# Kernel optimization log

Hardware: AMD Instinct MI355X
Metric: run time of the kernel (lower is better)

## Reference

```python
import jax, jax.numpy as jnp
import numpy as np

# 4-bit symmetric narrow-range weight quant (Brevitas Int-WeightPerTensorFloat style)
# and 4-bit unsigned activation quant after ReLU (QuantReLU style), with
# straight-through rounding so the same code is valid for the bwd reference.

W_QMAX = 7.0    # 2**(4-1)-1, narrow range symmetric int4: [-7, 7]
A_QMAX = 15.0   # unsigned 4-bit: [0, 15]
EPS = 1e-8


def _round_ste(x):
    return x + jax.lax.stop_gradient(jnp.round(x) - x)


def quant_weight(W):
    # per-tensor scale from max abs value
    scale = jnp.max(jnp.abs(W)) / W_QMAX + EPS
    q = jnp.clip(_round_ste(W / scale), -W_QMAX, W_QMAX)
    return q * scale


def quant_relu(x, scale):
    # ReLU fused with unsigned 4-bit quant/dequant, per-tensor learned scale
    q = jnp.clip(_round_ste(jax.nn.relu(x) / scale), 0.0, A_QMAX)
    return q * scale


def setup_inputs() -> dict:
    key = jax.random.key(0)
    k = jax.random.split(key, 4)
    B = 65536
    x = jax.random.normal(k[0], (B, 28, 28), dtype=jnp.float32)
    W1 = jax.random.normal(k[1], (512, 784), dtype=jnp.float32) * 0.05
    W2 = jax.random.normal(k[2], (512, 512), dtype=jnp.float32) * 0.05
    W3 = jax.random.normal(k[3], (10, 512), dtype=jnp.float32) * 0.05
    s1 = jnp.float32(1.0)  # QuantReLU activation scales (learned params)
    s2 = jnp.float32(1.0)
    return {"x": x, "W1": W1, "W2": W2, "W3": W3, "s1": s1, "s2": s2}


def reference(x, W1, W2, W3, s1, s2):
    h = x.reshape(x.shape[0], -1)                       # flatten [B, 784]
    h = h @ quant_weight(W1).T                          # QuantLinear 784->512
    h = quant_relu(h, s1)                               # QuantReLU
    h = h @ quant_weight(W2).T                          # QuantLinear 512->512
    h = quant_relu(h, s2)                               # QuantReLU
    logits = h @ quant_weight(W3).T                     # QuantLinear 512->10
    return logits
```

## Files before the change

### kernel.cpp

```cpp
#include <hip/hip_runtime.h>
#include <hip/hip_fp16.h>

typedef _Float16 f16;
typedef _Float16 f16x4 __attribute__((ext_vector_type(4)));
typedef _Float16 f16x8 __attribute__((ext_vector_type(8)));
typedef float f32x4 __attribute__((ext_vector_type(4)));
typedef int i32x4 __attribute__((ext_vector_type(4)));

#define MFMA16(a, b, c) __builtin_amdgcn_mfma_f32_16x16x32_f16((a), (b), (c), 0, 0, 0)
#define MFMAI8(a, b, c) __builtin_amdgcn_mfma_i32_16x16x64_i8((a), (b), (c), 0, 0, 0)

#define FLAG_CAP (1024 * 1024)
#define FLAG_TOL 1e-3f

__device__ __forceinline__ void gld16(const void* g, void* l) {
    __builtin_amdgcn_global_load_lds(
        (const __attribute__((address_space(1))) unsigned int*)g,
        (__attribute__((address_space(3))) unsigned int*)l,
        16, 0, 0);
}


__global__ void k_zero(float* p, int* cnt) {
    if (threadIdx.x < 3) p[threadIdx.x] = 0.f;
    if (threadIdx.x == 3) { cnt[0] = 0; cnt[1] = 0; }
}

__global__ void k_absmax(const float* __restrict__ w, int n, float* __restrict__ out) {
    float m = 0.f;
    int stride = gridDim.x * blockDim.x;
    for (int i = blockIdx.x * blockDim.x + threadIdx.x; i < n; i += stride)
        m = fmaxf(m, fabsf(w[i]));
    #pragma unroll
    for (int o = 32; o > 0; o >>= 1) m = fmaxf(m, __shfl_down(m, o));
    __shared__ float sm[4];
    int lane = threadIdx.x & 63, wv = threadIdx.x >> 6;
    if (lane == 0) sm[wv] = m;
    __syncthreads();
    if (threadIdx.x == 0) {
        float mm = fmaxf(fmaxf(sm[0], sm[1]), fmaxf(sm[2], sm[3]));
        atomicMax((unsigned int*)out, __float_as_uint(mm));
    }
}

__global__ void k_quantw1(const float* __restrict__ w, const float* __restrict__ wmax,
                          f16* __restrict__ q1, float* __restrict__ wdq,
                          f16* __restrict__ q1h) {
    int i = blockIdx.x * blockDim.x + threadIdx.x;
    if (i >= 512 * 832) return;
    int n = i / 832, k = i - n * 832;
    float v = 0.f;
    if (k < 784) {
        float s = wmax[0] / 7.0f + 1e-8f;
        v = rintf(w[n * 784 + k] / s);
        v = fminf(fmaxf(v, -7.f), 7.f);
        q1[n * 784 + k] = (f16)v;
        wdq[n * 784 + k] = v * s;
    }
    q1h[(size_t)n * 832 + k] = (f16)v;
}

__global__ void k_quantw2(const float* __restrict__ w, const float* __restrict__ wmax,
                          signed char* __restrict__ q, float* __restrict__ wdq, int n) {
    float s = wmax[0] / 7.0f + 1e-8f;
    int i = blockIdx.x * blockDim.x + threadIdx.x;
    if (i < n) {
        float v = rintf(w[i] / s);
        v = fminf(fmaxf(v, -7.f), 7.f);
        q[i] = (signed char)v;
        if (wdq) wdq[i] = v * s;
    }
}

__global__ void k_quantw3(const float* __restrict__ w, const float* __restrict__ wmax,
                          signed char* __restrict__ q) {
    float s = wmax[0] / 7.0f + 1e-8f;
    int i = blockIdx.x * blockDim.x + threadIdx.x;
    if (i < 16 * 512) {
        float v = 0.f;
        if (i < 10 * 512) {
            v = rintf(w[i] / s);
            v = fminf(fmaxf(v, -7.f), 7.f);
        }
        q[i] = (signed char)v;
    }
}


__global__ void k_prep(const float* __restrict__ X, f16* __restrict__ Xs) {
    int row = blockIdx.x;
    int p = threadIdx.x;
    if (p >= 208) return;
    f16x4 h0 = (f16x4){0, 0, 0, 0}, h1 = (f16x4){0, 0, 0, 0};
    if (p < 196) {
        float4 v = *reinterpret_cast<const float4*>(X + (size_t)row * 784 + p * 4);
        float vv[4] = {v.x, v.y, v.z, v.w};
        #pragma unroll
        for (int j = 0; j < 4; ++j) {
            f16 c0 = (f16)vv[j];
            h0[j] = c0;
            h1[j] = (f16)(vv[j] - (float)c0);
        }
    }
    *reinterpret_cast<f16x4*>(Xs + (size_t)row * 1664 + p * 4) = h0;
    *reinterpret_cast<f16x4*>(Xs + (size_t)row * 1664 + 832 + p * 4) = h1;
}


__global__ __launch_bounds__(256, 3) void k_gemm1h(
    const f16* __restrict__ A, const f16* __restrict__ B,
    const float* __restrict__ wmax, const float* __restrict__ s1p,
    signed char* __restrict__ A1, int* __restrict__ flagCnt, unsigned* __restrict__ flagList)
{
    constexpr int KA = 1664;
    constexpr int KB = 832;
    constexpr int NT = 13;
    __shared__ __align__(16) f16 Ah[128 * 64];
    __shared__ __align__(16) f16 Al[128 * 64];
    __shared__ __align__(16) f16 Bt[128 * 64];

    const int t = threadIdx.x;
    const int lane = t & 63, w = t >> 6;
    const int wr = w >> 1, wc = w & 1;

    const int bid = blockIdx.x;
    const int lg = (bid & 7) * 256 + (bid >> 3);
    const int n0 = (lg & 3) * 128;
    const int row0 = (lg >> 2) * 128;

    f32x4 acc[4][4];
    #pragma unroll
    for (int m = 0; m < 4; ++m)
        #pragma unroll
        for (int n = 0; n < 4; ++n) acc[m][n] = (f32x4){0.f, 0.f, 0.f, 0.f};

    const int lr = lane >> 3;
    const int lc = (((lane & 7) ^ (lane >> 3)) * 8);
    const f16* Ahb = A + (size_t)(row0 + lr) * KA + lc;
    const f16* Alb = A + (size_t)(row0 + lr) * KA + 832 + lc;
    const f16* Bb  = B + (size_t)(n0 + lr) * KB + lc;

    for (int tt = 0; tt < NT; ++tt) {
        const int k0 = tt * 64;
        #pragma unroll
        for (int i = 0; i < 4; ++i) {
            int ch = w * 4 + i;
            gld16(Ahb + (size_t)ch * 8 * KA + k0, &Ah[ch * 512]);
            gld16(Alb + (size_t)ch * 8 * KA + k0, &Al[ch * 512]);
            gld16(Bb  + (size_t)ch * 8 * KB + k0, &Bt[ch * 512]);
        }
        __syncthreads();

        #pragma unroll
        for (int kk = 0; kk < 2; ++kk) {
            int kb = kk * 32 + (lane >> 4) * 8;
            int ksw = kb ^ ((lane & 7) << 3);
            f16x8 bf[4], fh[4], fl[4];
            #pragma unroll
            for (int n = 0; n < 4; ++n)
                bf[n] = *reinterpret_cast<const f16x8*>(&Bt[(wc * 64 + n * 16 + (lane & 15)) * 64 + ksw]);
            #pragma unroll
            for (int m = 0; m < 4; ++m) {
                fh[m] = *reinterpret_cast<const f16x8*>(&Ah[(wr * 64 + m * 16 + (lane & 15)) * 64 + ksw]);
                fl[m] = *reinterpret_cast<const f16x8*>(&Al[(wr * 64 + m * 16 + (lane & 15)) * 64 + ksw]);
            }
            #pragma unroll
            for (int m = 0; m < 4; ++m)
                #pragma unroll
                for (int n = 0; n < 4; ++n) {
                    acc[m][n] = MFMA16(fh[m], bf[n], acc[m][n]);
                    acc[m][n] = MFMA16(fl[m], bf[n], acc[m][n]);
                }
        }
        __syncthreads();
    }

    float sw = wmax[0] / 7.0f + 1e-8f;
    float s1v = s1p[0];
    #pragma unroll
    for (int m = 0; m < 4; ++m)
        #pragma unroll
        for (int n = 0; n < 4; ++n)
            #pragma unroll
            for (int j = 0; j < 4; ++j) {
                int row = row0 + wr * 64 + m * 16 + (lane >> 4) * 4 + j;
                int col = n0 + wc * 64 + n * 16 + (lane & 15);
                float h = sw * acc[m][n][j];
                float r = fmaxf(h, 0.f) / s1v;
                float qv = fminf(rintf(r), 15.f);
                A1[(size_t)row * 512 + col] = (signed char)qv;
                float fr = r - floorf(r);
                if (fabsf(fr - 0.5f) < FLAG_TOL) {
                    int p = atomicAdd(flagCnt, 1);
                    if (p < FLAG_CAP) flagList[p] = (unsigned)(row * 512 + col);
                }
            }
}


__global__ __launch_bounds__(256, 4) void k_gemm2i(
    const signed char* __restrict__ A, const signed char* __restrict__ B,
    const float* __restrict__ wmax, const float* __restrict__ s1p, const float* __restrict__ s2p,
    signed char* __restrict__ A2, int* __restrict__ flagCnt, unsigned* __restrict__ flagList)
{
    constexpr int KP = 512;
    constexpr int NT = 4;
    __shared__ __align__(16) signed char As[128 * 128];
    __shared__ __align__(16) signed char Bs[128 * 128];

    const int t = threadIdx.x;
    const int lane = t & 63, w = t >> 6;
    const int wr = w >> 1, wc = w & 1;

    const int bid = blockIdx.x;
    const int lg = (bid & 7) * 256 + (bid >> 3);
    const int n0 = (lg & 3) * 128;
    const int row0 = (lg >> 2) * 128;

    i32x4 acc[4][4];
    #pragma unroll
    for (int m = 0; m < 4; ++m)
        #pragma unroll
        for (int n = 0; n < 4; ++n) acc[m][n] = (i32x4){0, 0, 0, 0};

    const int lr = lane >> 3;
    const int lcb = (((lane & 7) ^ (lane >> 3)) * 16);
    const signed char* Ab = A + (size_t)(row0 + lr) * KP + lcb;
    const signed char* Bb = B + (size_t)(n0 + lr) * KP + lcb;

    for (int tt = 0; tt < NT; ++tt) {
        const int k0 = tt * 128;
        #pragma unroll
        for (int i = 0; i < 4; ++i) {
            int ch = w * 4 + i;
            gld16(Ab + (size_t)ch * 8 * KP + k0, &As[ch * 1024]);
            gld16(Bb + (size_t)ch * 8 * KP + k0, &Bs[ch * 1024]);
        }
        __syncthreads();

        #pragma unroll
        for (int kk = 0; kk < 2; ++kk) {
            int sl = kk * 4 + (lane >> 4);
            int slw = (sl ^ (lane & 7)) * 16;
            i32x4 bf[4], af[4];
            #pragma unroll
            for (int n = 0; n < 4; ++n)
                bf[n] = *reinterpret_cast<const i32x4*>(&Bs[(wc * 64 + n * 16 + (lane & 15)) * 128 + slw]);
            #pragma unroll
            for (int m = 0; m < 4; ++m)
                af[m] = *reinterpret_cast<const i32x4*>(&As[(wr * 64 + m * 16 + (lane & 15)) * 128 + slw]);
            #pragma unroll
            for (int m = 0; m < 4; ++m)
                #pragma unroll
                for (int n = 0; n < 4; ++n)
                    acc[m][n] = MFMAI8(af[m], bf[n], acc[m][n]);
        }
        __syncthreads();
    }

    double cs = (double)s1p[0] * (double)(wmax[0] / 7.0f + 1e-8f);
    double s2v = (double)s2p[0];
    #pragma unroll
    for (int m = 0; m < 4; ++m)
        #pragma unroll
        for (int n = 0; n < 4; ++n)
            #pragma unroll
            for (int j = 0; j < 4; ++j) {
                int row = row0 + wr * 64 + m * 16 + (lane >> 4) * 4 + j;
                int col = n0 + wc * 64 + n * 16 + (lane & 15);
                double r = fmax((double)acc[m][n][j] * cs, 0.0) / s2v;
                double qv = fmin(rint(r), 15.0);
                A2[(size_t)row * 512 + col] = (signed char)qv;
                double fr = r - floor(r);
                if (fabs(fr - 0.5) < (double)FLAG_TOL && r < 16.0) {
                    int p = atomicAdd(flagCnt, 1);
                    if (p < FLAG_CAP) flagList[p] = (unsigned)(row * 512 + col);
                }
            }
}


__global__ __launch_bounds__(256) void k_gemm1s(
    const float* __restrict__ X, const f16* __restrict__ Q1,
    const float* __restrict__ wmax, const float* __restrict__ s1p,
    signed char* __restrict__ A1, int* __restrict__ flagCnt, unsigned* __restrict__ flagList)
{
    __shared__ __align__(16) f16 As0[128][72];
    __shared__ __align__(16) f16 As1[128][72];
    __shared__ __align__(16) f16 Bs[128][72];

    const int t = threadIdx.x;
    const int row0 = blockIdx.y * 128;
    const int n0 = blockIdx.x * 128;
    const int lane = t & 63, wv = t >> 6;
    const int wr = wv >> 1, wc = wv & 1;

    f32x4 acc[4][4];
    #pragma unroll
    for (int m = 0; m < 4; ++m)
        #pragma unroll
        for (int n = 0; n < 4; ++n) acc[m][n] = (f32x4){0.f, 0.f, 0.f, 0.f};

    for (int k0 = 0; k0 < 784; k0 += 64) {
        #pragma unroll
        for (int i = 0; i < 8; ++i) {
            int f = t + 256 * i;
            int r = f >> 4, c = f & 15;
            int gk = k0 + c * 4;
            float4 v = make_float4(0.f, 0.f, 0.f, 0.f);
            if (gk < 784)
                v = *reinterpret_cast<const float4*>(X + (size_t)(row0 + r) * 784 + gk);
            float vv[4] = {v.x, v.y, v.z, v.w};
            f16x4 h0, h1;
            #pragma unroll
            for (int j = 0; j < 4; ++j) {
                f16 c0 = (f16)vv[j];
                h0[j] = c0;
                h1[j] = (f16)(vv[j] - (float)c0);
            }
            *reinterpret_cast<f16x4*>(&As0[r][c * 4]) = h0;
            *reinterpret_cast<f16x4*>(&As1[r][c * 4]) = h1;
        }
        #pragma unroll
        for (int i = 0; i < 4; ++i) {
            int f = t + 256 * i;
            int r = f >> 3, c = f & 7;
            int gk = k0 + c * 8;
            uint4 u = make_uint4(0u, 0u, 0u, 0u);
            if (gk < 784)
                u = *reinterpret_cast<const uint4*>(Q1 + (size_t)(n0 + r) * 784 + gk);
            *reinterpret_cast<uint4*>(&Bs[r][c * 8]) = u;
        }
        __syncthreads();

        #pragma unroll
        for (int kk = 0; kk < 2; ++kk) {
            int kb = kk * 32 + (lane >> 4) * 8;
            f16x8 bf[4], a0[4], a1f[4];
            #pragma unroll
            for (int n = 0; n < 4; ++n)
                bf[n] = *reinterpret_cast<const f16x8*>(&Bs[wc * 64 + n * 16 + (lane & 15)][kb]);
            #pragma unroll
            for (int m = 0; m < 4; ++m) {
                a0[m]  = *reinterpret_cast<const f16x8*>(&As0[wr * 64 + m * 16 + (lane & 15)][kb]);
                a1f[m] = *reinterpret_cast<const f16x8*>(&As1[wr * 64 + m * 16 + (lane & 15)][kb]);
            }
            #pragma unroll
            for (int m = 0; m < 4; ++m)
                #pragma unroll
                for (int n = 0; n < 4; ++n) {
                    acc[m][n] = MFMA16(a0[m],  bf[n], acc[m][n]);
                    acc[m][n] = MFMA16(a1f[m], bf[n], acc[m][n]);
                }
        }
        __syncthreads();
    }

    float sw = wmax[0] / 7.0f + 1e-8f;
    float s1v = s1p[0];
    #pragma unroll
    for (int m = 0; m < 4; ++m)
        #pragma unroll
        for (int n = 0; n < 4; ++n)
            #pragma unroll
            for (int j = 0; j < 4; ++j) {
                int row = row0 + wr * 64 + m * 16 + (lane >> 4) * 4 + j;
                int col = n0 + wc * 64 + n * 16 + (lane & 15);
                float h = sw * acc[m][n][j];
                float r = fmaxf(h, 0.f) / s1v;
                float qv = fminf(rintf(r), 15.f);
                A1[(size_t)row * 512 + col] = (signed char)qv;
                float fr = r - floorf(r);
                if (fabsf(fr - 0.5f) < FLAG_TOL) {
                    int p = atomicAdd(flagCnt, 1);
                    if (p < FLAG_CAP) flagList[p] = (unsigned)(row * 512 + col);
                }
            }
}


__global__ void k_fixup1(const float* __restrict__ X, const float* __restrict__ W1dq,
                         const float* __restrict__ s1p,
                         const int* __restrict__ flagCnt, const unsigned* __restrict__ flagList,
                         signed char* __restrict__ A1)
{
    int tid = blockIdx.x * blockDim.x + threadIdx.x;
    int nthr = gridDim.x * blockDim.x;
    int n = flagCnt[0];
    if (n > FLAG_CAP) n = FLAG_CAP;
    float s1 = s1p[0];
    for (int i = tid; i < n; i += nthr) {
        unsigned idx = flagList[i];
        int row = (int)(idx >> 9), col = (int)(idx & 511);
        const float* xr = X + (size_t)row * 784;
        const float* wr = W1dq + (size_t)col * 784;
        float acc = 0.f;
        for (int k = 0; k < 784; ++k)
            acc = fmaf(xr[k], wr[k], acc);
        float tq = fmaxf(acc, 0.f) / s1;
        float code = fminf(rintf(tq), 15.f);
        A1[(size_t)row * 512 + col] = (signed char)code;
    }
}

__global__ void k_fixup2(const signed char* __restrict__ A1, const float* __restrict__ W2dq,
                         const float* __restrict__ s1p, const float* __restrict__ s2p,
                         const int* __restrict__ flagCnt, const unsigned* __restrict__ flagList,
                         signed char* __restrict__ A2)
{
    int tid = blockIdx.x * blockDim.x + threadIdx.x;
    int nthr = gridDim.x * blockDim.x;
    int n = flagCnt[0];
    if (n > FLAG_CAP) n = FLAG_CAP;
    float s1 = s1p[0], s2 = s2p[0];
    for (int i = tid; i < n; i += nthr) {
        unsigned idx = flagList[i];
        int row = (int)(idx >> 9), col = (int)(idx & 511);
        const signed char* ar = A1 + (size_t)row * 512;
        const float* wr = W2dq + (size_t)col * 512;
        float acc = 0.f;
        for (int k = 0; k < 512; ++k) {
            float adq = (float)ar[k] * s1;
            acc = fmaf(adq, wr[k], acc);
        }
        float tq = fmaxf(acc, 0.f) / s2;
        float code = fminf(rintf(tq), 15.f);
        A2[(size_t)row * 512 + col] = (signed char)code;
    }
}


__global__ __launch_bounds__(256) void k_gemm3i(
    const signed char* __restrict__ A2, const signed char* __restrict__ Q3,
    const float* __restrict__ wmax, const float* __restrict__ s2p,
    float* __restrict__ Out)
{
    __shared__ __align__(16) signed char As[256][80];
    __shared__ __align__(16) signed char Bs[16][80];

    const int t = threadIdx.x;
    const int row0 = blockIdx.x * 256;
    const int lane = t & 63, wv = t >> 6;

    i32x4 acc[4];
    #pragma unroll
    for (int m = 0; m < 4; ++m) acc[m] = (i32x4){0, 0, 0, 0};

    for (int k0 = 0; k0 < 512; k0 += 64) {
        #pragma unroll
        for (int i = 0; i < 4; ++i) {
            int f = t + 256 * i;
            int r = f >> 2, c = f & 3;
            *reinterpret_cast<uint4*>(&As[r][c * 16]) =
                *reinterpret_cast<const uint4*>(A2 + (size_t)(row0 + r) * 512 + k0 + c * 16);
        }
        if (t < 64) {
            int r = t >> 2, c = t & 3;
            *reinterpret_cast<uint4*>(&Bs[r][c * 16]) =
                *reinterpret_cast<const uint4*>(Q3 + (size_t)r * 512 + k0 + c * 16);
        }
        __syncthreads();

        i32x4 bf = *reinterpret_cast<const i32x4*>(&Bs[lane & 15][(lane >> 4) * 16]);
        #pragma unroll
        for (int m = 0; m < 4; ++m) {
            i32x4 af = *reinterpret_cast<const i32x4*>(&As[wv * 64 + m * 16 + (lane & 15)][(lane >> 4) * 16]);
            acc[m] = MFMAI8(af, bf, acc[m]);
        }
        __syncthreads();
    }

    double cs = (double)s2p[0] * (double)(wmax[0] / 7.0f + 1e-8f);
    #pragma unroll
    for (int m = 0; m < 4; ++m)
        #pragma unroll
        for (int j = 0; j < 4; ++j) {
            int row = row0 + wv * 64 + m * 16 + (lane >> 4) * 4 + j;
            int col = lane & 15;
            if (col < 10)
                Out[(size_t)row * 10 + col] = (float)((double)acc[m][j] * cs);
        }
}


extern "C" void kernel_launch(void* const* d_in, const int* in_sizes, int n_in,
                              void* d_out, int out_size, void* d_ws, size_t ws_size,
                              hipStream_t stream)
{
    (void)in_sizes; (void)n_in; (void)out_size;

    const float* X  = (const float*)d_in[0];
    const float* W1 = (const float*)d_in[1];
    const float* W2 = (const float*)d_in[2];
    const float* W3 = (const float*)d_in[3];
    const float* s1 = (const float*)d_in[4];
    const float* s2 = (const float*)d_in[5];
    float* Out = (float*)d_out;

    char* ws = (char*)d_ws;
    float* maxes        = (float*)ws;
    int*   cnts         = (int*)(ws + 16);
    f16*   q1           = (f16*)(ws + 4096);
    signed char* q2i    = (signed char*)(ws + (size_t)(1u << 20));
    signed char* q3i    = (signed char*)(ws + (size_t)(1u << 20) + 300000);
    f16*   q1h          = (f16*)(ws + (size_t)(2u << 20));
    float* w1dq         = (float*)(ws + (size_t)(4u << 20));
    float* w2dq         = (float*)(ws + (size_t)(6u << 20));
    signed char* a1     = (signed char*)(ws + (size_t)(8u << 20));
    signed char* a2     = (signed char*)(ws + (size_t)(40u << 20));
    unsigned* fl1       = (unsigned*)(ws + (size_t)(72u << 20));
    unsigned* fl2       = (unsigned*)(ws + (size_t)(76u << 20));
    f16*   Xs           = (f16*)(ws + (size_t)(80u << 20));

    const bool big = ws_size >= ((size_t)300 << 20);

    k_zero<<<1, 64, 0, stream>>>(maxes, cnts);
    k_absmax<<<256, 256, 0, stream>>>(W1, 512 * 784, maxes + 0);
    k_absmax<<<256, 256, 0, stream>>>(W2, 512 * 512, maxes + 1);
    k_absmax<<<8, 256, 0, stream>>>(W3, 10 * 512, maxes + 2);
    k_quantw1<<<(512 * 832 + 255) / 256, 256, 0, stream>>>(W1, maxes + 0, q1, w1dq, q1h);
    k_quantw2<<<(512 * 512 + 255) / 256, 256, 0, stream>>>(W2, maxes + 1, q2i, w2dq, 512 * 512);
    k_quantw3<<<(16 * 512 + 255) / 256, 256, 0, stream>>>(W3, maxes + 2, q3i);

    if (big) {
        k_prep<<<65536, 256, 0, stream>>>(X, Xs);
        k_gemm1h<<<2048, 256, 0, stream>>>(Xs, q1h, maxes + 0, s1, a1, cnts + 0, fl1);
    } else {
        k_gemm1s<<<dim3(4, 512), 256, 0, stream>>>(X, q1, maxes + 0, s1, a1, cnts + 0, fl1);
    }
    k_fixup1<<<512, 256, 0, stream>>>(X, w1dq, s1, cnts + 0, fl1, a1);
    k_gemm2i<<<2048, 256, 0, stream>>>(a1, q2i, maxes + 1, s1, s2, a2, cnts + 1, fl2);
    k_fixup2<<<512, 256, 0, stream>>>(a1, w2dq, s1, s2, cnts + 1, fl2, a2);
    k_gemm3i<<<256, 256, 0, stream>>>(a2, q3i, maxes + 2, s2, Out);
}
```

Baseline: 669.5 us.

## Fuse fp16 split of X into GEMM1 and widen both GEMMs to full-N tiles

Removes the separate prep kernel that wrote a split hi/lo fp16 copy of X to global memory. GEMM1 now loads fp32 X directly, converts it to hi/lo fp16 in registers and writes it into double-buffered, swizzled LDS, prefetching the next K tile while the MFMAs run. Both GEMM1 and the int8 GEMM2 now use 512-thread blocks that compute a 128x512 output tile, so each A tile is loaded once instead of four times, and A is double-buffered with explicit waitcnt and barrier control. The costs are a large LDS footprint that limits occupancy, more accumulator registers per thread, and dropping the small-workspace fallback path.

Result: faster. 624.4 us (-6.7%).

```diff
diff --git a/kernel.cpp b/kernel.cpp
--- a/kernel.cpp
+++ b/kernel.cpp
@@ -12,6 +12,9 @@
 
 #define FLAG_CAP (1024 * 1024)
 #define FLAG_TOL 1e-3f
+
+#define SBAR()   __builtin_amdgcn_s_barrier()
+#define SCHEDB() __builtin_amdgcn_sched_barrier(0)
 
 __device__ __forceinline__ void gld16(const void* g, void* l) {
     __builtin_amdgcn_global_load_lds(
@@ -44,8 +47,7 @@
 }
 
 __global__ void k_quantw1(const float* __restrict__ w, const float* __restrict__ wmax,
-                          f16* __restrict__ q1, float* __restrict__ wdq,
-                          f16* __restrict__ q1h) {
+                          float* __restrict__ wdq, f16* __restrict__ q1h) {
     int i = blockIdx.x * blockDim.x + threadIdx.x;
     if (i >= 512 * 832) return;
     int n = i / 832, k = i - n * 832;
@@ -54,7 +56,6 @@
         float s = wmax[0] / 7.0f + 1e-8f;
         v = rintf(w[n * 784 + k] / s);
         v = fminf(fmaxf(v, -7.f), 7.f);
-        q1[n * 784 + k] = (f16)v;
         wdq[n * 784 + k] = v * s;
     }
     q1h[(size_t)n * 832 + k] = (f16)v;
@@ -87,92 +88,108 @@
 }
 
 
-__global__ void k_prep(const float* __restrict__ X, f16* __restrict__ Xs) {
-    int row = blockIdx.x;
-    int p = threadIdx.x;
-    if (p >= 208) return;
-    f16x4 h0 = (f16x4){0, 0, 0, 0}, h1 = (f16x4){0, 0, 0, 0};
-    if (p < 196) {
-        float4 v = *reinterpret_cast<const float4*>(X + (size_t)row * 784 + p * 4);
-        float vv[4] = {v.x, v.y, v.z, v.w};
-        #pragma unroll
-        for (int j = 0; j < 4; ++j) {
-            f16 c0 = (f16)vv[j];
-            h0[j] = c0;
-            h1[j] = (f16)(vv[j] - (float)c0);
-        }
-    }
-    *reinterpret_cast<f16x4*>(Xs + (size_t)row * 1664 + p * 4) = h0;
-    *reinterpret_cast<f16x4*>(Xs + (size_t)row * 1664 + 832 + p * 4) = h1;
-}
-
-
-__global__ __launch_bounds__(256, 3) void k_gemm1h(
-    const f16* __restrict__ A, const f16* __restrict__ B,
+__global__ __launch_bounds__(512, 2) void k_gemm1F(
+    const float* __restrict__ X, const f16* __restrict__ B,
     const float* __restrict__ wmax, const float* __restrict__ s1p,
     signed char* __restrict__ A1, int* __restrict__ flagCnt, unsigned* __restrict__ flagList)
 {
-    constexpr int KA = 1664;
-    constexpr int KB = 832;
     constexpr int NT = 13;
-    __shared__ __align__(16) f16 Ah[128 * 64];
-    __shared__ __align__(16) f16 Al[128 * 64];
-    __shared__ __align__(16) f16 Bt[128 * 64];
+    __shared__ __align__(16) f16 Ah[2][128 * 64];
+    __shared__ __align__(16) f16 Al[2][128 * 64];
+    __shared__ __align__(16) f16 Bt[512 * 64];
 
     const int t = threadIdx.x;
     const int lane = t & 63, w = t >> 6;
-    const int wr = w >> 1, wc = w & 1;
-
-    const int bid = blockIdx.x;
-    const int lg = (bid & 7) * 256 + (bid >> 3);
-    const int n0 = (lg & 3) * 128;
-    const int row0 = (lg >> 2) * 128;
-
-    f32x4 acc[4][4];
+    const int wr = w >> 2, wc = w & 3;
+    const int l15 = lane & 15, l4 = lane >> 4;
+    const int row0 = blockIdx.x * 128;
+
+    f32x4 acc[4][8];
     #pragma unroll
     for (int m = 0; m < 4; ++m)
         #pragma unroll
-        for (int n = 0; n < 4; ++n) acc[m][n] = (f32x4){0.f, 0.f, 0.f, 0.f};
+        for (int n = 0; n < 8; ++n) acc[m][n] = (f32x4){0.f, 0.f, 0.f, 0.f};
 
     const int lr = lane >> 3;
-    const int lc = (((lane & 7) ^ (lane >> 3)) * 8);
-    const f16* Ahb = A + (size_t)(row0 + lr) * KA + lc;
-    const f16* Alb = A + (size_t)(row0 + lr) * KA + 832 + lc;
-    const f16* Bb  = B + (size_t)(n0 + lr) * KB + lc;
-
+    const int lc = ((lane & 7) ^ lr) * 8;
+    const f16* Bb = B + (size_t)lr * 832 + lc;
+
+    float4 av[4];
+    auto LOADA = [&](int tn) {
+        #pragma unroll
+        for (int i = 0; i < 4; ++i) {
+            int f = t + 512 * i;
+            int r = f >> 4, s = f & 15;
+            int gk = tn * 64 + s * 4;
+            av[i] = make_float4(0.f, 0.f, 0.f, 0.f);
+            if (gk < 784)
+                av[i] = *reinterpret_cast<const float4*>(X + (size_t)(row0 + r) * 784 + gk);
+        }
+    };
+    auto WRITEA = [&](int buf) {
+        #pragma unroll
+        for (int i = 0; i < 4; ++i) {
+            int f = t + 512 * i;
+            int r = f >> 4, s = f & 15;
+            float vv[4] = {av[i].x, av[i].y, av[i].z, av[i].w};
+            f16x4 h0, h1;
+            #pragma unroll
+            for (int j = 0; j < 4; ++j) {
+                f16 c0 = (f16)vv[j];
+                h0[j] = c0;
+                h1[j] = (f16)(vv[j] - (float)c0);
+            }
+            int ad = r * 64 + ((s * 4) ^ ((r & 7) << 3));
+            *reinterpret_cast<f16x4*>(&Ah[buf][ad]) = h0;
+            *reinterpret_cast<f16x4*>(&Al[buf][ad]) = h1;
+        }
+    };
+
+    LOADA(0);
+    asm volatile("s_waitcnt vmcnt(0)" ::: "memory");
+    WRITEA(0);
+
+    int cur = 0;
     for (int tt = 0; tt < NT; ++tt) {
-        const int k0 = tt * 64;
-        #pragma unroll
-        for (int i = 0; i < 4; ++i) {
-            int ch = w * 4 + i;
-            gld16(Ahb + (size_t)ch * 8 * KA + k0, &Ah[ch * 512]);
-            gld16(Alb + (size_t)ch * 8 * KA + k0, &Al[ch * 512]);
-            gld16(Bb  + (size_t)ch * 8 * KB + k0, &Bt[ch * 512]);
-        }
-        __syncthreads();
+        #pragma unroll
+        for (int i = 0; i < 8; ++i) {
+            int ch = w * 8 + i;
+            gld16(Bb + (size_t)ch * 8 * 832 + tt * 64, &Bt[ch * 512]);
+        }
+        SCHEDB();
+        int tn = (tt + 1 < NT) ? tt + 1 : tt;
+        LOADA(tn);
+        SCHEDB();
+        asm volatile("s_waitcnt vmcnt(4)" ::: "memory");
+        asm volatile("s_waitcnt lgkmcnt(0)" ::: "memory");
+        SBAR();
 
         #pragma unroll
         for (int kk = 0; kk < 2; ++kk) {
-            int kb = kk * 32 + (lane >> 4) * 8;
+            int kb = kk * 32 + l4 * 8;
             int ksw = kb ^ ((lane & 7) << 3);
-            f16x8 bf[4], fh[4], fl[4];
-            #pragma unroll
-            for (int n = 0; n < 4; ++n)
-                bf[n] = *reinterpret_cast<const f16x8*>(&Bt[(wc * 64 + n * 16 + (lane & 15)) * 64 + ksw]);
+            f16x8 fh[4], fl_[4], bf[8];
             #pragma unroll
             for (int m = 0; m < 4; ++m) {
-                fh[m] = *reinterpret_cast<const f16x8*>(&Ah[(wr * 64 + m * 16 + (lane & 15)) * 64 + ksw]);
-                fl[m] = *reinterpret_cast<const f16x8*>(&Al[(wr * 64 + m * 16 + (lane & 15)) * 64 + ksw]);
+                fh[m]  = *reinterpret_cast<const f16x8*>(&Ah[cur][(wr * 64 + m * 16 + l15) * 64 + ksw]);
+                fl_[m] = *reinterpret_cast<const f16x8*>(&Al[cur][(wr * 64 + m * 16 + l15) * 64 + ksw]);
             }
+            #pragma unroll
+            for (int n = 0; n < 8; ++n)
+                bf[n] = *reinterpret_cast<const f16x8*>(&Bt[(wc * 128 + n * 16 + l15) * 64 + ksw]);
             #pragma unroll
             for (int m = 0; m < 4; ++m)
                 #pragma unroll
-                for (int n = 0; n < 4; ++n) {
-                    acc[m][n] = MFMA16(fh[m], bf[n], acc[m][n]);
-                    acc[m][n] = MFMA16(fl[m], bf[n], acc[m][n]);
+                for (int n = 0; n < 8; ++n) {
+                    acc[m][n] = MFMA16(fh[m],  bf[n], acc[m][n]);
+                    acc[m][n] = MFMA16(fl_[m], bf[n], acc[m][n]);
                 }
         }
-        __syncthreads();
+
+        asm volatile("s_waitcnt vmcnt(0)" ::: "memory");
+        WRITEA(cur ^ 1);
+        SBAR();
+        cur ^= 1;
     }
 
     float sw = wmax[0] / 7.0f + 1e-8f;
@@ -180,11 +197,11 @@
     #pragma unroll
     for (int m = 0; m < 4; ++m)
         #pragma unroll
-        for (int n = 0; n < 4; ++n)
+        for (int n = 0; n < 8; ++n)
             #pragma unroll
             for (int j = 0; j < 4; ++j) {
-                int row = row0 + wr * 64 + m * 16 + (lane >> 4) * 4 + j;
-                int col = n0 + wc * 64 + n * 16 + (lane & 15);
+                int row = row0 + wr * 64 + m * 16 + l4 * 4 + j;
+                int col = wc * 128 + n * 16 + l15;
                 float h = sw * acc[m][n][j];
                 float r = fmaxf(h, 0.f) / s1v;
                 float qv = fminf(rintf(r), 15.f);
@@ -198,64 +215,76 @@
 }
 
 
-__global__ __launch_bounds__(256, 4) void k_gemm2i(
+__global__ __launch_bounds__(512, 2) void k_gemm2F(
     const signed char* __restrict__ A, const signed char* __restrict__ B,
     const float* __restrict__ wmax, const float* __restrict__ s1p, const float* __restrict__ s2p,
     signed char* __restrict__ A2, int* __restrict__ flagCnt, unsigned* __restrict__ flagList)
 {
-    constexpr int KP = 512;
     constexpr int NT = 4;
-    __shared__ __align__(16) signed char As[128 * 128];
-    __shared__ __align__(16) signed char Bs[128 * 128];
+    __shared__ __align__(16) signed char As[2][128 * 128];
+    __shared__ __align__(16) signed char Bs[512 * 128];
 
     const int t = threadIdx.x;
     const int lane = t & 63, w = t >> 6;
-    const int wr = w >> 1, wc = w & 1;
-
-    const int bid = blockIdx.x;
-    const int lg = (bid & 7) * 256 + (bid >> 3);
-    const int n0 = (lg & 3) * 128;
-    const int row0 = (lg >> 2) * 128;
-
-    i32x4 acc[4][4];
+    const int wr = w >> 2, wc = w & 3;
+    const int l15 = lane & 15, l4 = lane >> 4;
+    const int row0 = blockIdx.x * 128;
+
+    i32x4 acc[4][8];
     #pragma unroll
     for (int m = 0; m < 4; ++m)
         #pragma unroll
-        for (int n = 0; n < 4; ++n) acc[m][n] = (i32x4){0, 0, 0, 0};
+        for (int n = 0; n < 8; ++n) acc[m][n] = (i32x4){0, 0, 0, 0};
 
     const int lr = lane >> 3;
-    const int lcb = (((lane & 7) ^ (lane >> 3)) * 16);
-    const signed char* Ab = A + (size_t)(row0 + lr) * KP + lcb;
-    const signed char* Bb = B + (size_t)(n0 + lr) * KP + lcb;
-
+    const int lcb = ((lane & 7) ^ lr) * 16;
+    const signed char* Ab = A + (size_t)(row0 + lr) * 512 + lcb;
+    const signed char* Bb = B + (size_t)lr * 512 + lcb;
+
+    #pragma unroll
+    for (int i = 0; i < 2; ++i) {
+        int ch = w * 2 + i;
+        gld16(Ab + (size_t)ch * 8 * 512, &As[0][ch * 1024]);
+    }
+
+    int cur = 0;
     for (int tt = 0; tt < NT; ++tt) {
-        const int k0 = tt * 128;
-        #pragma unroll
-        for (int i = 0; i < 4; ++i) {
-            int ch = w * 4 + i;
-            gld16(Ab + (size_t)ch * 8 * KP + k0, &As[ch * 1024]);
-            gld16(Bb + (size_t)ch * 8 * KP + k0, &Bs[ch * 1024]);
-        }
-        __syncthreads();
+        #pragma unroll
+        for (int i = 0; i < 8; ++i) {
+            int ch = w * 8 + i;
+            gld16(Bb + (size_t)ch * 8 * 512 + tt * 128, &Bs[ch * 1024]);
+        }
+        SCHEDB();
+        int tn = (tt + 1 < NT) ? tt + 1 : tt;
+        #pragma unroll
+        for (int i = 0; i < 2; ++i) {
+            int ch = w * 2 + i;
+            gld16(Ab + (size_t)ch * 8 * 512 + tn * 128, &As[cur ^ 1][ch * 1024]);
+        }
+        SCHEDB();
+        asm volatile("s_waitcnt vmcnt(2)" ::: "memory");
+        SBAR();
 
         #pragma unroll
         for (int kk = 0; kk < 2; ++kk) {
-            int sl = kk * 4 + (lane >> 4);
+            int sl = kk * 4 + l4;
             int slw = (sl ^ (lane & 7)) * 16;
-            i32x4 bf[4], af[4];
-            #pragma unroll
-            for (int n = 0; n < 4; ++n)
-                bf[n] = *reinterpret_cast<const i32x4*>(&Bs[(wc * 64 + n * 16 + (lane & 15)) * 128 + slw]);
+            i32x4 af[4], bf[8];
             #pragma unroll
             for (int m = 0; m < 4; ++m)
-                af[m] = *reinterpret_cast<const i32x4*>(&As[(wr * 64 + m * 16 + (lane & 15)) * 128 + slw]);
+                af[m] = *reinterpret_cast<const i32x4*>(&As[cur][(wr * 64 + m * 16 + l15) * 128 + slw]);
+            #pragma unroll
+            for (int n = 0; n < 8; ++n)
+                bf[n] = *reinterpret_cast<const i32x4*>(&Bs[(wc * 128 + n * 16 + l15) * 128 + slw]);
             #pragma unroll
             for (int m = 0; m < 4; ++m)
                 #pragma unroll
-                for (int n = 0; n < 4; ++n)
+                for (int n = 0; n < 8; ++n)
                     acc[m][n] = MFMAI8(af[m], bf[n], acc[m][n]);
         }
-        __syncthreads();
+
+        SBAR();
+        cur ^= 1;
     }
 
     double cs = (double)s1p[0] * (double)(wmax[0] / 7.0f + 1e-8f);
@@ -263,115 +292,16 @@
     #pragma unroll
     for (int m = 0; m < 4; ++m)
         #pragma unroll
-        for (int n = 0; n < 4; ++n)
+        for (int n = 0; n < 8; ++n)
             #pragma unroll
             for (int j = 0; j < 4; ++j) {
-                int row = row0 + wr * 64 + m * 16 + (lane >> 4) * 4 + j;
-                int col = n0 + wc * 64 + n * 16 + (lane & 15);
+                int row = row0 + wr * 64 + m * 16 + l4 * 4 + j;
+                int col = wc * 128 + n * 16 + l15;
                 double r = fmax((double)acc[m][n][j] * cs, 0.0) / s2v;
                 double qv = fmin(rint(r), 15.0);
                 A2[(size_t)row * 512 + col] = (signed char)qv;
                 double fr = r - floor(r);
                 if (fabs(fr - 0.5) < (double)FLAG_TOL && r < 16.0) {
-                    int p = atomicAdd(flagCnt, 1);
-                    if (p < FLAG_CAP) flagList[p] = (unsigned)(row * 512 + col);
-                }
-            }
-}
-
-
-__global__ __launch_bounds__(256) void k_gemm1s(
-    const float* __restrict__ X, const f16* __restrict__ Q1,
-    const float* __restrict__ wmax, const float* __restrict__ s1p,
-    signed char* __restrict__ A1, int* __restrict__ flagCnt, unsigned* __restrict__ flagList)
-{
-    __shared__ __align__(16) f16 As0[128][72];
-    __shared__ __align__(16) f16 As1[128][72];
-    __shared__ __align__(16) f16 Bs[128][72];
-
-    const int t = threadIdx.x;
-    const int row0 = blockIdx.y * 128;
-    const int n0 = blockIdx.x * 128;
-    const int lane = t & 63, wv = t >> 6;
-    const int wr = wv >> 1, wc = wv & 1;
-
-    f32x4 acc[4][4];
-    #pragma unroll
-    for (int m = 0; m < 4; ++m)
-        #pragma unroll
-        for (int n = 0; n < 4; ++n) acc[m][n] = (f32x4){0.f, 0.f, 0.f, 0.f};
-
-    for (int k0 = 0; k0 < 784; k0 += 64) {
-        #pragma unroll
-        for (int i = 0; i < 8; ++i) {
-            int f = t + 256 * i;
-            int r = f >> 4, c = f & 15;
-            int gk = k0 + c * 4;
-            float4 v = make_float4(0.f, 0.f, 0.f, 0.f);
-            if (gk < 784)
-                v = *reinterpret_cast<const float4*>(X + (size_t)(row0 + r) * 784 + gk);
-            float vv[4] = {v.x, v.y, v.z, v.w};
-            f16x4 h0, h1;
-            #pragma unroll
-            for (int j = 0; j < 4; ++j) {
-                f16 c0 = (f16)vv[j];
-                h0[j] = c0;
-                h1[j] = (f16)(vv[j] - (float)c0);
-            }
-            *reinterpret_cast<f16x4*>(&As0[r][c * 4]) = h0;
-            *reinterpret_cast<f16x4*>(&As1[r][c * 4]) = h1;
-        }
-        #pragma unroll
-        for (int i = 0; i < 4; ++i) {
-            int f = t + 256 * i;
-            int r = f >> 3, c = f & 7;
-            int gk = k0 + c * 8;
-            uint4 u = make_uint4(0u, 0u, 0u, 0u);
-            if (gk < 784)
-                u = *reinterpret_cast<const uint4*>(Q1 + (size_t)(n0 + r) * 784 + gk);
-            *reinterpret_cast<uint4*>(&Bs[r][c * 8]) = u;
-        }
-        __syncthreads();
-
-        #pragma unroll
-        for (int kk = 0; kk < 2; ++kk) {
-            int kb = kk * 32 + (lane >> 4) * 8;
-            f16x8 bf[4], a0[4], a1f[4];
-            #pragma unroll
-            for (int n = 0; n < 4; ++n)
-                bf[n] = *reinterpret_cast<const f16x8*>(&Bs[wc * 64 + n * 16 + (lane & 15)][kb]);
-            #pragma unroll
-            for (int m = 0; m < 4; ++m) {
-                a0[m]  = *reinterpret_cast<const f16x8*>(&As0[wr * 64 + m * 16 + (lane & 15)][kb]);
-                a1f[m] = *reinterpret_cast<const f16x8*>(&As1[wr * 64 + m * 16 + (lane & 15)][kb]);
-            }
-            #pragma unroll
-            for (int m = 0; m < 4; ++m)
-                #pragma unroll
-                for (int n = 0; n < 4; ++n) {
-                    acc[m][n] = MFMA16(a0[m],  bf[n], acc[m][n]);
-                    acc[m][n] = MFMA16(a1f[m], bf[n], acc[m][n]);
-                }
-        }
-        __syncthreads();
-    }
-
-    float sw = wmax[0] / 7.0f + 1e-8f;
-    float s1v = s1p[0];
-    #pragma unroll
-    for (int m = 0; m < 4; ++m)
-        #pragma unroll
-        for (int n = 0; n < 4; ++n)
-            #pragma unroll
-            for (int j = 0; j < 4; ++j) {
-                int row = row0 + wr * 64 + m * 16 + (lane >> 4) * 4 + j;
-                int col = n0 + wc * 64 + n * 16 + (lane & 15);
-                float h = sw * acc[m][n][j];
-                float r = fmaxf(h, 0.f) / s1v;
-                float qv = fminf(rintf(r), 15.f);
-                A1[(size_t)row * 512 + col] = (signed char)qv;
-                float fr = r - floorf(r);
-                if (fabsf(fr - 0.5f) < FLAG_TOL) {
                     int p = atomicAdd(flagCnt, 1);
                     if (p < FLAG_CAP) flagList[p] = (unsigned)(row * 512 + col);
                 }
@@ -487,7 +417,7 @@
                               void* d_out, int out_size, void* d_ws, size_t ws_size,
                               hipStream_t stream)
 {
-    (void)in_sizes; (void)n_in; (void)out_size;
+    (void)in_sizes; (void)n_in; (void)out_size; (void)ws_size;
 
     const float* X  = (const float*)d_in[0];
     const float* W1 = (const float*)d_in[1];
@@ -498,38 +428,29 @@
     float* Out = (float*)d_out;
 
     char* ws = (char*)d_ws;
-    float* maxes        = (float*)ws;
-    int*   cnts         = (int*)(ws + 16);
-    f16*   q1           = (f16*)(ws + 4096);
-    signed char* q2i    = (signed char*)(ws + (size_t)(1u << 20));
-    signed char* q3i    = (signed char*)(ws + (size_t)(1u << 20) + 300000);
-    f16*   q1h          = (f16*)(ws + (size_t)(2u << 20));
-    float* w1dq         = (float*)(ws + (size_t)(4u << 20));
-    float* w2dq         = (float*)(ws + (size_t)(6u << 20));
-    signed char* a1     = (signed char*)(ws + (size_t)(8u << 20));
-    signed char* a2     = (signed char*)(ws + (size_t)(40u << 20));
-    unsigned* fl1       = (unsigned*)(ws + (size_t)(72u << 20));
-    unsigned* fl2       = (unsigned*)(ws + (size_t)(76u << 20));
-    f16*   Xs           = (f16*)(ws + (size_t)(80u << 20));
-
-    const bool big = ws_size >= ((size_t)300 << 20);
+    float* maxes     = (float*)ws;
+    int*   cnts      = (int*)(ws + 16);
+    f16*   q1h       = (f16*)(ws + (size_t)(1u << 20));
+    float* w1dq      = (float*)(ws + (size_t)(2u << 20));
+    float* w2dq      = (float*)(ws + (size_t)(4u << 20));
+    signed char* q2i = (signed char*)(ws + (size_t)(6u << 20));
+    signed char* q3i = (signed char*)(ws + (size_t)(6u << 20) + 300000);
+    signed char* a1  = (signed char*)(ws + (size_t)(8u << 20));
+    signed char* a2  = (signed char*)(ws + (size_t)(40u << 20));
+    unsigned* fl1    = (unsigned*)(ws + (size_t)(72u << 20));
+    unsigned* fl2    = (unsigned*)(ws + (size_t)(76u << 20));
 
     k_zero<<<1, 64, 0, stream>>>(maxes, cnts);
     k_absmax<<<256, 256, 0, stream>>>(W1, 512 * 784, maxes + 0);
     k_absmax<<<256, 256, 0, stream>>>(W2, 512 * 512, maxes + 1);
     k_absmax<<<8, 256, 0, stream>>>(W3, 10 * 512, maxes + 2);
-    k_quantw1<<<(512 * 832 + 255) / 256, 256, 0, stream>>>(W1, maxes + 0, q1, w1dq, q1h);
+    k_quantw1<<<(512 * 832 + 255) / 256, 256, 0, stream>>>(W1, maxes + 0, w1dq, q1h);
     k_quantw2<<<(512 * 512 + 255) / 256, 256, 0, stream>>>(W2, maxes + 1, q2i, w2dq, 512 * 512);
     k_quantw3<<<(16 * 512 + 255) / 256, 256, 0, stream>>>(W3, maxes + 2, q3i);
 
-    if (big) {
-        k_prep<<<65536, 256, 0, stream>>>(X, Xs);
-        k_gemm1h<<<2048, 256, 0, stream>>>(Xs, q1h, maxes + 0, s1, a1, cnts + 0, fl1);
-    } else {
-        k_gemm1s<<<dim3(4, 512), 256, 0, stream>>>(X, q1, maxes + 0, s1, a1, cnts + 0, fl1);
-    }
+    k_gemm1F<<<512, 512, 0, stream>>>(X, q1h, maxes + 0, s1, a1, cnts + 0, fl1);
     k_fixup1<<<512, 256, 0, stream>>>(X, w1dq, s1, cnts + 0, fl1, a1);
-    k_gemm2i<<<2048, 256, 0, stream>>>(a1, q2i, maxes + 1, s1, s2, a2, cnts + 1, fl2);
+    k_gemm2F<<<512, 512, 0, stream>>>(a1, q2i, maxes + 1, s1, s2, a2, cnts + 1, fl2);
     k_fixup2<<<512, 256, 0, stream>>>(a1, w2dq, s1, s2, cnts + 1, fl2, a2);
     k_gemm3i<<<256, 256, 0, stream>>>(a2, q3i, maxes + 2, s2, Out);
 }
```
